# Performance work log

Hardware: AMD Instinct MI355X
Metric: run time of the kernel (lower is better)

Reference implementation:

```python
import jax, jax.numpy as jnp
import numpy as np

HIDDEN = 1024
N_HEADS = 16
HEAD_DIM = 64
BS, QS = 4, 2048
NEG = -60000.0


def setup_inputs() -> dict:
    key = jax.random.key(0)
    k1, k2, k3, k4 = jax.random.split(key, 4)
    x = jax.random.normal(k1, (BS, QS, HIDDEN), dtype=jnp.float32)
    att_mask = jax.random.randint(k2, (BS, QS, QS), 0, 2).astype(bool)
    # nn.Linear(hidden, out, bias=False): store as [in, out] so y = x @ W
    W_qk = jax.random.normal(k3, (HIDDEN, 2 * N_HEADS * HEAD_DIM), dtype=jnp.float32) / np.sqrt(HIDDEN)
    W_v = jax.random.normal(k4, (HIDDEN, N_HEADS), dtype=jnp.float32) / np.sqrt(HIDDEN)
    return {"x": x, "att_mask": att_mask, "W_qk": W_qk, "W_v": W_v}


def reference(x, att_mask, W_qk, W_v):
    # mem is None -> c = x, ks == qs
    bs, qs, _ = x.shape
    n_heads = W_v.shape[1]
    head_dim = W_qk.shape[1] // (2 * n_heads)
    att_scale = 1.0 / head_dim ** 0.5

    qk = x @ W_qk                                   # [b, k, 2*n*d]
    query, key = jnp.split(qk, 2, axis=-1)
    value = x @ W_v                                 # [b, k, n]  (per-head V dim is 1)

    q = query.reshape(bs, qs, n_heads, head_dim)
    k = key.reshape(bs, qs, n_heads, head_dim)

    # att_score: [b, q, k, n]
    scores = jnp.einsum('bqnd,bknd->bqkn', q, k) * att_scale
    scores = jnp.where(att_mask[..., None], NEG, scores)  # True = masked
    prob = jax.nn.softmax(scores, axis=2)           # softmax over k
    # attended bqnd with d=1, then .sum(2) over heads -> [b, q, 1]
    attended = jnp.einsum('bqkn,bkn->bqn', prob, value)
    out = attended.sum(-1, keepdims=True)           # [b, q, 1]

    padded_mask = att_mask[:, -1]                   # [b, k] == [b, q]
    out = jnp.where(padded_mask[..., None], NEG, out)
    out = jax.nn.sigmoid(out)
    # torch version also returns out.nonzero() (data-dependent shape); omitted for jit.
    return out
```

## Files before the change

kernel.cpp:

```cpp
#include <hip/hip_runtime.h>

typedef unsigned short u16;
typedef unsigned int u32;
typedef unsigned long long u64;
typedef __attribute__((ext_vector_type(8))) short bf16x8;
typedef __attribute__((ext_vector_type(4))) float f32x4;

#define BATCH 4
#define SEQ 2048
#define HID 1024
#define NHEAD 16
#define HDIM 64
#define C1 0.18033688011112042f

#if __has_builtin(__builtin_amdgcn_exp2f)
#define EXP2(x) __builtin_amdgcn_exp2f(x)
#else
#define EXP2(x) exp2f(x)
#endif

__device__ __forceinline__ u16 f2bf(float f) {
    u32 u = __builtin_bit_cast(u32, f);
    u += 0x7fffu + ((u >> 16) & 1u);
    return (u16)(u >> 16);
}

__device__ __forceinline__ void gl_lds16(const void* g, void* l) {
    __builtin_amdgcn_global_load_lds((const __attribute__((address_space(1))) u32*)g,
                                     (__attribute__((address_space(3))) u32*)l, 16, 0, 0);
}

__global__ __launch_bounds__(1024) void flagk(const unsigned char* mask, int* flag) {
    __shared__ int any;
    if (threadIdx.x == 0) any = 0;
    __syncthreads();
    const uint4* m4 = (const uint4*)mask;
    u32 acc = 0;
#pragma unroll
    for (int j = 0; j < 4; ++j) {
        uint4 v = m4[threadIdx.x + j * 1024];
        acc |= (v.x | v.y | v.z | v.w) & 0xFFFFFF00u;
    }
    if (acc) atomicOr(&any, 1);
    __syncthreads();
    if (threadIdx.x == 0) *flag = (any == 0) ? 1 : 0;
}

__global__ void convx(const float* __restrict__ x, u16* __restrict__ xb) {
    int i = blockIdx.x * 256 + threadIdx.x;
    float4 v = ((const float4*)x)[i];
    ushort4 o;
    o.x = f2bf(v.x); o.y = f2bf(v.y); o.z = f2bf(v.z); o.w = f2bf(v.w);
    ((ushort4*)xb)[i] = o;
}

__global__ __launch_bounds__(256) void transw(const float* __restrict__ W, u16* __restrict__ wT) {
    __shared__ float t[32][33];
    int nb = blockIdx.x & 63, hb = blockIdx.x >> 6;
    int tx = threadIdx.x & 31, ty = threadIdx.x >> 5;
#pragma unroll
    for (int i = 0; i < 4; ++i)
        t[ty + i * 8][tx] = W[(size_t)(hb * 32 + ty + i * 8) * 2048 + nb * 32 + tx];
    __syncthreads();
#pragma unroll
    for (int i = 0; i < 4; ++i)
        wT[(size_t)(nb * 32 + ty + i * 8) * 1024 + hb * 32 + tx] = f2bf(t[tx][ty + i * 8]);
}

__global__ __launch_bounds__(256) void value_gemm(const float* __restrict__ x,
                                                  const float* __restrict__ Wv,
                                                  float* __restrict__ vT) {
    __shared__ float xs[16 * 1024];
    int s0 = blockIdx.x * 16;
    const float4* xg = (const float4*)(x + (size_t)s0 * HID);
    float4* xd = (float4*)xs;
    for (int i = threadIdx.x; i < 4096; i += 256) xd[i] = xg[i];
    __syncthreads();
    int sl = threadIdx.x >> 4, n = threadIdx.x & 15;
    float acc = 0.f;
    for (int hh = 0; hh < HID; ++hh) acc += xs[sl * HID + hh] * Wv[hh * 16 + n];
    int s = s0 + sl;
    int b = s >> 11, q = s & 2047;
    vT[((size_t)b * 16 + n) * SEQ + q] = acc;
}

__global__ void bitpack(const void* __restrict__ mask, const int* __restrict__ flag,
                        u64* __restrict__ bm) {
    int base = blockIdx.x * 2048 + threadIdx.x;
    int fl = *flag;
#pragma unroll
    for (int k = 0; k < 8; ++k) {
        int i = base + k * 256;
        int v;
        if (fl) v = ((const int*)mask)[i];
        else    v = ((const unsigned char*)mask)[i];
        u64 bits = __ballot(v == 0);
        if ((threadIdx.x & 63) == 0) bm[i >> 6] = bits;
    }
}

__global__ __launch_bounds__(256) void proj_gemm(const u16* __restrict__ xb,
                                                 const u16* __restrict__ wT,
                                                 u16* __restrict__ qkb) {
    __shared__ __align__(16) u16 As[2][128 * 64];
    __shared__ __align__(16) u16 Bs[2][128 * 64];
    int tid = threadIdx.x, w = tid >> 6, lane = tid & 63;
    int g = lane >> 4, l15 = lane & 15;
    int bid = blockIdx.x;
    int swz = (bid & 7) * 128 + (bid >> 3);
    int bm = swz >> 4, bn = swz & 15;
    int m0 = bm * 128, n0 = bn * 128;
    int wm = w >> 1, wn = w & 1;
    const u16* asrc[4];
    const u16* bsrc[4];
#pragma unroll
    for (int j = 0; j < 4; ++j) {
        int ci = (w * 4 + j) * 64 + lane;
        int row = ci >> 3, cl = (ci & 7) ^ (row & 7);
        asrc[j] = xb + (size_t)(m0 + row) * HID + cl * 8;
        bsrc[j] = wT + (size_t)(n0 + row) * HID + cl * 8;
    }
    f32x4 acc[4][4] = {};
#pragma unroll
    for (int j = 0; j < 4; ++j) {
        gl_lds16(asrc[j], &As[0][(w * 4 + j) * 512]);
        gl_lds16(bsrc[j], &Bs[0][(w * 4 + j) * 512]);
        asrc[j] += 64; bsrc[j] += 64;
    }
    for (int kt = 0; kt < 16; ++kt) {
        int cur = kt & 1;
        asm volatile("s_waitcnt vmcnt(0)" ::: "memory");
        __builtin_amdgcn_s_barrier();
        __builtin_amdgcn_sched_barrier(0);
        if (kt < 15) {
#pragma unroll
            for (int j = 0; j < 4; ++j) {
                gl_lds16(asrc[j], &As[cur ^ 1][(w * 4 + j) * 512]);
                gl_lds16(bsrc[j], &Bs[cur ^ 1][(w * 4 + j) * 512]);
                asrc[j] += 64; bsrc[j] += 64;
            }
        }
#pragma unroll
        for (int kk = 0; kk < 2; ++kk) {
            bf16x8 af[4], bf[4];
#pragma unroll
            for (int m = 0; m < 4; ++m) {
                int row = wm * 64 + m * 16 + l15;
                int cp = (kk * 4 + g) ^ (row & 7);
                af[m] = *(const bf16x8*)&As[cur][row * 64 + cp * 8];
            }
#pragma unroll
            for (int n = 0; n < 4; ++n) {
                int row = wn * 64 + n * 16 + l15;
                int cp = (kk * 4 + g) ^ (row & 7);
                bf[n] = *(const bf16x8*)&Bs[cur][row * 64 + cp * 8];
            }
#pragma unroll
            for (int m = 0; m < 4; ++m)
#pragma unroll
                for (int n = 0; n < 4; ++n)
                    acc[m][n] = __builtin_amdgcn_mfma_f32_16x16x32_bf16(af[m], bf[n], acc[m][n], 0, 0, 0);
        }
    }
    float scale = (bn < 8) ? C1 : 1.0f;
#pragma unroll
    for (int m = 0; m < 4; ++m)
#pragma unroll
        for (int n = 0; n < 4; ++n)
#pragma unroll
            for (int r = 0; r < 4; ++r) {
                int row = m0 + wm * 64 + m * 16 + g * 4 + r;
                int col = n0 + wn * 64 + n * 16 + l15;
                qkb[(size_t)row * 2048 + col] = f2bf(acc[m][n][r] * scale);
            }
}

__global__ __launch_bounds__(512, 4) void attn(const u16* __restrict__ qkb,
                                               const float* __restrict__ vT,
                                               const u64* __restrict__ bmk,
                                               float* __restrict__ hatt) {
    __shared__ __align__(16) u16 Ks[3][64 * 64];
    __shared__ __align__(16) float Vh[2048];
    __shared__ __align__(16) float Tb[16][4];
    int tid = threadIdx.x, w = tid >> 6, lane = tid & 63;
    int g = lane >> 4, l15 = lane & 15, g4 = g * 4;
    int bid = blockIdx.x;
    int swzb = (bid & 7) * 64 + (bid >> 3);
    int qt = swzb & 7, h = (swzb >> 3) & 15, b = swzb >> 7;
    int q0 = qt * 256;
    if (tid < 64) Tb[tid >> 2][tid & 3] = (float)(((tid >> 2) >> (tid & 3)) & 1);
    int qA = q0 + w * 32 + l15, qB = qA + 16;
    const u16* qrowA = qkb + (size_t)(b * SEQ + qA) * 2048 + h * 64;
    const u16* qrowB = qkb + (size_t)(b * SEQ + qB) * 2048 + h * 64;
    bf16x8 qfA0 = *(const bf16x8*)(qrowA + g * 8);
    bf16x8 qfA1 = *(const bf16x8*)(qrowA + 32 + g * 8);
    bf16x8 qfB0 = *(const bf16x8*)(qrowB + g * 8);
    bf16x8 qfB1 = *(const bf16x8*)(qrowB + 32 + g * 8);
    gl_lds16(vT + ((size_t)b * 16 + h) * SEQ + tid * 4, &Vh[w * 256]);
    const u64* mrowA = bmk + ((size_t)b * SEQ + qA) * 32;
    const u64* mrowB = bmk + ((size_t)b * SEQ + qB) * 32;
    int srow = tid >> 3, scol = (tid & 7) ^ (srow & 7);
    const u16* ksrc = qkb + (size_t)(b * SEQ + srow) * 2048 + 1024 + h * 64 + scol * 8;
    u64 mA_cur = mrowA[0], mB_cur = mrowB[0];
    gl_lds16(ksrc, &Ks[0][w * 512]); ksrc += 64 * 2048;
    u64 mA_nxt = mrowA[1], mB_nxt = mrowB[1];
    gl_lds16(ksrc, &Ks[1][w * 512]); ksrc += 64 * 2048;
    int e0[4], e1[4];
#pragma unroll
    for (int cb = 0; cb < 4; ++cb) {
        int krow = cb * 16 + l15;
        e0[cb] = krow * 64 + ((g) ^ (krow & 7)) * 8;
        e1[cb] = krow * 64 + ((4 + g) ^ (krow & 7)) * 8;
    }
    float nmA0 = 0.f, nmA1 = 0.f, nmA2 = 0.f, nmA3 = 0.f;
    float dnA0 = 0.f, dnA1 = 0.f, dnA2 = 0.f, dnA3 = 0.f;
    float nmB0 = 0.f, nmB1 = 0.f, nmB2 = 0.f, nmB3 = 0.f;
    float dnB0 = 0.f, dnB1 = 0.f, dnB2 = 0.f, dnB3 = 0.f;
    asm volatile("s_waitcnt lgkmcnt(0)" ::: "memory");

    auto compute = [&](int kt) {
        const u16* kcur = &Ks[kt % 3][0];
        const float* vk = &Vh[kt * 64 + g4];
        u64 shA = mA_cur >> g4, shB = mB_cur >> g4;
        u32 aLo = (u32)shA, aHi = (u32)(shA >> 32);
        u32 bLo = (u32)shB, bHi = (u32)(shB >> 32);
        int idxA[4] = {(int)(aLo & 15), (int)((aLo >> 16) & 15),
                       (int)(aHi & 15), (int)((aHi >> 16) & 15)};
        int idxB[4] = {(int)(bLo & 15), (int)((bLo >> 16) & 15),
                       (int)(bHi & 15), (int)((bHi >> 16) & 15)};
#pragma unroll
        for (int cb = 0; cb < 4; ++cb) {
            bf16x8 kf0 = *(const bf16x8*)&kcur[e0[cb]];
            bf16x8 kf1 = *(const bf16x8*)&kcur[e1[cb]];
            f32x4 aA = {0.f, 0.f, 0.f, 0.f}, aB = {0.f, 0.f, 0.f, 0.f};
            aA = __builtin_amdgcn_mfma_f32_16x16x32_bf16(kf0, qfA0, aA, 0, 0, 0);
            aA = __builtin_amdgcn_mfma_f32_16x16x32_bf16(kf1, qfA1, aA, 0, 0, 0);
            aB = __builtin_amdgcn_mfma_f32_16x16x32_bf16(kf0, qfB0, aB, 0, 0, 0);
            aB = __builtin_amdgcn_mfma_f32_16x16x32_bf16(kf1, qfB1, aB, 0, 0, 0);
            const float4 mA4 = *(const float4*)&Tb[idxA[cb]][0];
            const float4 mB4 = *(const float4*)&Tb[idxB[cb]][0];
            const float4 vv = *(const float4*)&vk[cb * 16];
            float pA0 = EXP2(aA[0]) * mA4.x, pA1 = EXP2(aA[1]) * mA4.y;
            float pA2 = EXP2(aA[2]) * mA4.z, pA3 = EXP2(aA[3]) * mA4.w;
            float pB0 = EXP2(aB[0]) * mB4.x, pB1 = EXP2(aB[1]) * mB4.y;
            float pB2 = EXP2(aB[2]) * mB4.z, pB3 = EXP2(aB[3]) * mB4.w;
            dnA0 += pA0; dnA1 += pA1; dnA2 += pA2; dnA3 += pA3;
            dnB0 += pB0; dnB1 += pB1; dnB2 += pB2; dnB3 += pB3;
            nmA0 = fmaf(pA0, vv.x, nmA0); nmA1 = fmaf(pA1, vv.y, nmA1);
            nmA2 = fmaf(pA2, vv.z, nmA2); nmA3 = fmaf(pA3, vv.w, nmA3);
            nmB0 = fmaf(pB0, vv.x, nmB0); nmB1 = fmaf(pB1, vv.y, nmB1);
            nmB2 = fmaf(pB2, vv.z, nmB2); nmB3 = fmaf(pB3, vv.w, nmB3);
        }
    };

    for (int kt = 0; kt < 31; ++kt) {
        asm volatile("s_waitcnt vmcnt(3)" ::: "memory");
        __builtin_amdgcn_s_barrier();
        __builtin_amdgcn_sched_barrier(0);
        u64 mA_n2, mB_n2;
        if (kt < 30) {
            mA_n2 = mrowA[kt + 2]; mB_n2 = mrowB[kt + 2];
            gl_lds16(ksrc, &Ks[(kt + 2) % 3][w * 512]); ksrc += 64 * 2048;
        } else { mA_n2 = 0; mB_n2 = 0; }
        compute(kt);
        mA_cur = mA_nxt; mB_cur = mB_nxt;
        mA_nxt = mA_n2; mB_nxt = mB_n2;
    }
    asm volatile("s_waitcnt vmcnt(0)" ::: "memory");
    __builtin_amdgcn_s_barrier();
    __builtin_amdgcn_sched_barrier(0);
    compute(31);

    float numA = (nmA0 + nmA1) + (nmA2 + nmA3);
    float denA = (dnA0 + dnA1) + (dnA2 + dnA3);
    float numB = (nmB0 + nmB1) + (nmB2 + nmB3);
    float denB = (dnB0 + dnB1) + (dnB2 + dnB3);
    numA += __shfl_xor(numA, 16); denA += __shfl_xor(denA, 16);
    numA += __shfl_xor(numA, 32); denA += __shfl_xor(denA, 32);
    numB += __shfl_xor(numB, 16); denB += __shfl_xor(denB, 16);
    numB += __shfl_xor(numB, 32); denB += __shfl_xor(denB, 32);
    if (g == 0) {
        hatt[((size_t)b * SEQ + qA) * 16 + h] = numA / denA;
        hatt[((size_t)b * SEQ + qB) * 16 + h] = numB / denB;
    }
}

__global__ void epi(const float* __restrict__ hatt, const void* __restrict__ mask,
                    const int* __restrict__ flag, float* __restrict__ out) {
    int i = blockIdx.x * 256 + threadIdx.x;
    int b = i >> 11, q = i & 2047;
    const float4* hp = (const float4*)(hatt + (size_t)i * 16);
    float t = 0.f;
#pragma unroll
    for (int j = 0; j < 4; ++j) {
        float4 u = hp[j];
        t += u.x + u.y + u.z + u.w;
    }
    size_t mi = ((size_t)b * SEQ + (SEQ - 1)) * SEQ + q;
    int m;
    if (*flag) m = ((const int*)mask)[mi];
    else       m = ((const unsigned char*)mask)[mi];
    out[i] = m ? 0.f : 1.f / (1.f + expf(-t));
}

extern "C" void kernel_launch(void* const* d_in, const int* in_sizes, int n_in,
                              void* d_out, int out_size, void* d_ws, size_t ws_size,
                              hipStream_t stream) {
    const float* x = (const float*)d_in[0];
    const void* mask = d_in[1];
    const float* Wqk = (const float*)d_in[2];
    const float* Wv = (const float*)d_in[3];
    float* out = (float*)d_out;
    char* ws = (char*)d_ws;
    u16* xb = (u16*)(ws + 0);
    u16* wT = (u16*)(ws + 16777216);
    u16* qkb = (u16*)(ws + 20971520);
    float* vT = (float*)(ws + 54525952);
    u64* bm = (u64*)(ws + 55050240);
    float* hatt = (float*)(ws + 0);
    int* flag = (int*)(ws + 57147392);

    flagk<<<1, 1024, 0, stream>>>((const unsigned char*)mask, flag);
    convx<<<8192, 256, 0, stream>>>(x, xb);
    transw<<<2048, 256, 0, stream>>>(Wqk, wT);
    value_gemm<<<512, 256, 0, stream>>>(x, Wv, vT);
    bitpack<<<8192, 256, 0, stream>>>(mask, flag, bm);
    proj_gemm<<<1024, 256, 0, stream>>>(xb, wT, qkb);
    attn<<<512, 512, 0, stream>>>(qkb, vT, bm, hatt);
    epi<<<32, 256, 0, stream>>>(hatt, mask, flag, out);
}
```

Before: 168.3 us.

## Fuse x bf16 conversion with value GEMM and halve attention query tile

After: 170.8 us. No clear change (+1.4%).

```diff
diff --git a/kernel.cpp b/kernel.cpp
--- a/kernel.cpp
+++ b/kernel.cpp
@@ -46,12 +46,36 @@
     if (threadIdx.x == 0) *flag = (any == 0) ? 1 : 0;
 }
 
-__global__ void convx(const float* __restrict__ x, u16* __restrict__ xb) {
-    int i = blockIdx.x * 256 + threadIdx.x;
-    float4 v = ((const float4*)x)[i];
-    ushort4 o;
-    o.x = f2bf(v.x); o.y = f2bf(v.y); o.z = f2bf(v.z); o.w = f2bf(v.w);
-    ((ushort4*)xb)[i] = o;
+__global__ __launch_bounds__(256) void convxv(const float* __restrict__ x,
+                                              const float* __restrict__ Wv,
+                                              u16* __restrict__ xb,
+                                              float* __restrict__ vT) {
+    __shared__ float xs[16 * 1024];
+    int s0 = blockIdx.x * 16;
+    const float4* xg = (const float4*)(x + (size_t)s0 * HID);
+    float4* xd = (float4*)xs;
+    ushort4* xo = (ushort4*)(xb + (size_t)s0 * HID);
+#pragma unroll
+    for (int j = 0; j < 16; ++j) {
+        int i = j * 256 + threadIdx.x;
+        float4 v = xg[i];
+        xd[i] = v;
+        ushort4 o;
+        o.x = f2bf(v.x); o.y = f2bf(v.y); o.z = f2bf(v.z); o.w = f2bf(v.w);
+        xo[i] = o;
+    }
+    __syncthreads();
+    int sl = threadIdx.x >> 4, n = threadIdx.x & 15;
+    const float4* xrow = (const float4*)&xs[sl * HID];
+    float acc = 0.f;
+    for (int h4 = 0; h4 < 256; ++h4) {
+        float4 xv = xrow[h4];
+        acc += xv.x * Wv[(h4 * 4 + 0) * 16 + n] + xv.y * Wv[(h4 * 4 + 1) * 16 + n]
+             + xv.z * Wv[(h4 * 4 + 2) * 16 + n] + xv.w * Wv[(h4 * 4 + 3) * 16 + n];
+    }
+    int s = s0 + sl;
+    int b = s >> 11, q = s & 2047;
+    vT[((size_t)b * 16 + n) * SEQ + q] = acc;
 }
 
 __global__ __launch_bounds__(256) void transw(const float* __restrict__ W, u16* __restrict__ wT) {
@@ -65,23 +89,6 @@
 #pragma unroll
     for (int i = 0; i < 4; ++i)
         wT[(size_t)(nb * 32 + ty + i * 8) * 1024 + hb * 32 + tx] = f2bf(t[tx][ty + i * 8]);
-}
-
-__global__ __launch_bounds__(256) void value_gemm(const float* __restrict__ x,
-                                                  const float* __restrict__ Wv,
-                                                  float* __restrict__ vT) {
-    __shared__ float xs[16 * 1024];
-    int s0 = blockIdx.x * 16;
-    const float4* xg = (const float4*)(x + (size_t)s0 * HID);
-    float4* xd = (float4*)xs;
-    for (int i = threadIdx.x; i < 4096; i += 256) xd[i] = xg[i];
-    __syncthreads();
-    int sl = threadIdx.x >> 4, n = threadIdx.x & 15;
-    float acc = 0.f;
-    for (int hh = 0; hh < HID; ++hh) acc += xs[sl * HID + hh] * Wv[hh * 16 + n];
-    int s = s0 + sl;
-    int b = s >> 11, q = s & 2047;
-    vT[((size_t)b * 16 + n) * SEQ + q] = acc;
 }
 
 __global__ void bitpack(const void* __restrict__ mask, const int* __restrict__ flag,
@@ -185,25 +192,21 @@
     int tid = threadIdx.x, w = tid >> 6, lane = tid & 63;
     int g = lane >> 4, l15 = lane & 15, g4 = g * 4;
     int bid = blockIdx.x;
-    int swzb = (bid & 7) * 64 + (bid >> 3);
-    int qt = swzb & 7, h = (swzb >> 3) & 15, b = swzb >> 7;
-    int q0 = qt * 256;
+    int bh = bid & 63, qt = bid >> 6;
+    int h = bh & 15, b = bh >> 4;
+    int q0 = qt * 128;
     if (tid < 64) Tb[tid >> 2][tid & 3] = (float)(((tid >> 2) >> (tid & 3)) & 1);
-    int qA = q0 + w * 32 + l15, qB = qA + 16;
-    const u16* qrowA = qkb + (size_t)(b * SEQ + qA) * 2048 + h * 64;
-    const u16* qrowB = qkb + (size_t)(b * SEQ + qB) * 2048 + h * 64;
-    bf16x8 qfA0 = *(const bf16x8*)(qrowA + g * 8);
-    bf16x8 qfA1 = *(const bf16x8*)(qrowA + 32 + g * 8);
-    bf16x8 qfB0 = *(const bf16x8*)(qrowB + g * 8);
-    bf16x8 qfB1 = *(const bf16x8*)(qrowB + 32 + g * 8);
+    int q = q0 + w * 16 + l15;
+    const u16* qrow = qkb + (size_t)(b * SEQ + q) * 2048 + h * 64;
+    bf16x8 qf0 = *(const bf16x8*)(qrow + g * 8);
+    bf16x8 qf1 = *(const bf16x8*)(qrow + 32 + g * 8);
     gl_lds16(vT + ((size_t)b * 16 + h) * SEQ + tid * 4, &Vh[w * 256]);
-    const u64* mrowA = bmk + ((size_t)b * SEQ + qA) * 32;
-    const u64* mrowB = bmk + ((size_t)b * SEQ + qB) * 32;
+    const u64* mrow = bmk + ((size_t)b * SEQ + q) * 32;
     int srow = tid >> 3, scol = (tid & 7) ^ (srow & 7);
     const u16* ksrc = qkb + (size_t)(b * SEQ + srow) * 2048 + 1024 + h * 64 + scol * 8;
-    u64 mA_cur = mrowA[0], mB_cur = mrowB[0];
+    u64 m_cur = mrow[0];
     gl_lds16(ksrc, &Ks[0][w * 512]); ksrc += 64 * 2048;
-    u64 mA_nxt = mrowA[1], mB_nxt = mrowB[1];
+    u64 m_nxt = mrow[1];
     gl_lds16(ksrc, &Ks[1][w * 512]); ksrc += 64 * 2048;
     int e0[4], e1[4];
 #pragma unroll
@@ -212,77 +215,61 @@
         e0[cb] = krow * 64 + ((g) ^ (krow & 7)) * 8;
         e1[cb] = krow * 64 + ((4 + g) ^ (krow & 7)) * 8;
     }
-    float nmA0 = 0.f, nmA1 = 0.f, nmA2 = 0.f, nmA3 = 0.f;
-    float dnA0 = 0.f, dnA1 = 0.f, dnA2 = 0.f, dnA3 = 0.f;
-    float nmB0 = 0.f, nmB1 = 0.f, nmB2 = 0.f, nmB3 = 0.f;
-    float dnB0 = 0.f, dnB1 = 0.f, dnB2 = 0.f, dnB3 = 0.f;
-    asm volatile("s_waitcnt lgkmcnt(0)" ::: "memory");
+    float nm0 = 0.f, nm1 = 0.f, nm2 = 0.f, nm3 = 0.f;
+    float dn0 = 0.f, dn1 = 0.f, dn2 = 0.f, dn3 = 0.f;
+    asm volatile("s_waitcnt vmcnt(0) lgkmcnt(0)" ::: "memory");
+    __builtin_amdgcn_s_barrier();
 
     auto compute = [&](int kt) {
         const u16* kcur = &Ks[kt % 3][0];
         const float* vk = &Vh[kt * 64 + g4];
-        u64 shA = mA_cur >> g4, shB = mB_cur >> g4;
-        u32 aLo = (u32)shA, aHi = (u32)(shA >> 32);
-        u32 bLo = (u32)shB, bHi = (u32)(shB >> 32);
-        int idxA[4] = {(int)(aLo & 15), (int)((aLo >> 16) & 15),
-                       (int)(aHi & 15), (int)((aHi >> 16) & 15)};
-        int idxB[4] = {(int)(bLo & 15), (int)((bLo >> 16) & 15),
-                       (int)(bHi & 15), (int)((bHi >> 16) & 15)};
+        u64 sh = m_cur >> g4;
+        u32 mlo = (u32)sh, mhi = (u32)(sh >> 32);
+        int idx[4] = {(int)(mlo & 15), (int)((mlo >> 16) & 15),
+                      (int)(mhi & 15), (int)((mhi >> 16) & 15)};
 #pragma unroll
         for (int cb = 0; cb < 4; ++cb) {
             bf16x8 kf0 = *(const bf16x8*)&kcur[e0[cb]];
             bf16x8 kf1 = *(const bf16x8*)&kcur[e1[cb]];
-            f32x4 aA = {0.f, 0.f, 0.f, 0.f}, aB = {0.f, 0.f, 0.f, 0.f};
-            aA = __builtin_amdgcn_mfma_f32_16x16x32_bf16(kf0, qfA0, aA, 0, 0, 0);
-            aA = __builtin_amdgcn_mfma_f32_16x16x32_bf16(kf1, qfA1, aA, 0, 0, 0);
-            aB = __builtin_amdgcn_mfma_f32_16x16x32_bf16(kf0, qfB0, aB, 0, 0, 0);
-            aB = __builtin_amdgcn_mfma_f32_16x16x32_bf16(kf1, qfB1, aB, 0, 0, 0);
-            const float4 mA4 = *(const float4*)&Tb[idxA[cb]][0];
-            const float4 mB4 = *(const float4*)&Tb[idxB[cb]][0];
+            f32x4 a = {0.f, 0.f, 0.f, 0.f};
+            a = __builtin_amdgcn_mfma_f32_16x16x32_bf16(kf0, qf0, a, 0, 0, 0);
+            a = __builtin_amdgcn_mfma_f32_16x16x32_bf16(kf1, qf1, a, 0, 0, 0);
+            const float4 m4 = *(const float4*)&Tb[idx[cb]][0];
             const float4 vv = *(const float4*)&vk[cb * 16];
-            float pA0 = EXP2(aA[0]) * mA4.x, pA1 = EXP2(aA[1]) * mA4.y;
-            float pA2 = EXP2(aA[2]) * mA4.z, pA3 = EXP2(aA[3]) * mA4.w;
-            float pB0 = EXP2(aB[0]) * mB4.x, pB1 = EXP2(aB[1]) * mB4.y;
-            float pB2 = EXP2(aB[2]) * mB4.z, pB3 = EXP2(aB[3]) * mB4.w;
-            dnA0 += pA0; dnA1 += pA1; dnA2 += pA2; dnA3 += pA3;
-            dnB0 += pB0; dnB1 += pB1; dnB2 += pB2; dnB3 += pB3;
-            nmA0 = fmaf(pA0, vv.x, nmA0); nmA1 = fmaf(pA1, vv.y, nmA1);
-            nmA2 = fmaf(pA2, vv.z, nmA2); nmA3 = fmaf(pA3, vv.w, nmA3);
-            nmB0 = fmaf(pB0, vv.x, nmB0); nmB1 = fmaf(pB1, vv.y, nmB1);
-            nmB2 = fmaf(pB2, vv.z, nmB2); nmB3 = fmaf(pB3, vv.w, nmB3);
+            float p0 = EXP2(a[0]) * m4.x;
+            float p1 = EXP2(a[1]) * m4.y;
+            float p2 = EXP2(a[2]) * m4.z;
+            float p3 = EXP2(a[3]) * m4.w;
+            dn0 += p0; dn1 += p1; dn2 += p2; dn3 += p3;
+            nm0 = fmaf(p0, vv.x, nm0);
+            nm1 = fmaf(p1, vv.y, nm1);
+            nm2 = fmaf(p2, vv.z, nm2);
+            nm3 = fmaf(p3, vv.w, nm3);
         }
     };
 
     for (int kt = 0; kt < 31; ++kt) {
-        asm volatile("s_waitcnt vmcnt(3)" ::: "memory");
+        asm volatile("s_waitcnt vmcnt(2)" ::: "memory");
         __builtin_amdgcn_s_barrier();
         __builtin_amdgcn_sched_barrier(0);
-        u64 mA_n2, mB_n2;
+        u64 m_n2 = 0;
         if (kt < 30) {
-            mA_n2 = mrowA[kt + 2]; mB_n2 = mrowB[kt + 2];
+            m_n2 = mrow[kt + 2];
             gl_lds16(ksrc, &Ks[(kt + 2) % 3][w * 512]); ksrc += 64 * 2048;
-        } else { mA_n2 = 0; mB_n2 = 0; }
+        }
         compute(kt);
-        mA_cur = mA_nxt; mB_cur = mB_nxt;
-        mA_nxt = mA_n2; mB_nxt = mB_n2;
+        m_cur = m_nxt; m_nxt = m_n2;
     }
     asm volatile("s_waitcnt vmcnt(0)" ::: "memory");
     __builtin_amdgcn_s_barrier();
     __builtin_amdgcn_sched_barrier(0);
     compute(31);
 
-    float numA = (nmA0 + nmA1) + (nmA2 + nmA3);
-    float denA = (dnA0 + dnA1) + (dnA2 + dnA3);
-    float numB = (nmB0 + nmB1) + (nmB2 + nmB3);
-    float denB = (dnB0 + dnB1) + (dnB2 + dnB3);
-    numA += __shfl_xor(numA, 16); denA += __shfl_xor(denA, 16);
-    numA += __shfl_xor(numA, 32); denA += __shfl_xor(denA, 32);
-    numB += __shfl_xor(numB, 16); denB += __shfl_xor(denB, 16);
-    numB += __shfl_xor(numB, 32); denB += __shfl_xor(denB, 32);
-    if (g == 0) {
-        hatt[((size_t)b * SEQ + qA) * 16 + h] = numA / denA;
-        hatt[((size_t)b * SEQ + qB) * 16 + h] = numB / denB;
-    }
+    float num = (nm0 + nm1) + (nm2 + nm3);
+    float den = (dn0 + dn1) + (dn2 + dn3);
+    num += __shfl_xor(num, 16); den += __shfl_xor(den, 16);
+    num += __shfl_xor(num, 32); den += __shfl_xor(den, 32);
+    if (g == 0) hatt[((size_t)b * SEQ + q) * 16 + h] = num / den;
 }
 
 __global__ void epi(const float* __restrict__ hatt, const void* __restrict__ mask,
@@ -321,11 +308,10 @@
     int* flag = (int*)(ws + 57147392);
 
     flagk<<<1, 1024, 0, stream>>>((const unsigned char*)mask, flag);
-    convx<<<8192, 256, 0, stream>>>(x, xb);
+    convxv<<<512, 256, 0, stream>>>(x, Wv, xb, vT);
     transw<<<2048, 256, 0, stream>>>(Wqk, wT);
-    value_gemm<<<512, 256, 0, stream>>>(x, Wv, vT);
     bitpack<<<8192, 256, 0, stream>>>(mask, flag, bm);
     proj_gemm<<<1024, 256, 0, stream>>>(xb, wT, qkb);
-    attn<<<512, 512, 0, stream>>>(qkb, vT, bm, hatt);
+    attn<<<1024, 512, 0, stream>>>(qkb, vT, bm, hatt);
     epi<<<32, 256, 0, stream>>>(hatt, mask, flag, out);
 }
```

## Fuse bf16 conversion with value GEMM; load K directly to registers in attention

Applied to the files above, without the earlier changes.

New measurement: 379.7 us. 126% more time.

```diff
diff --git a/kernel.cpp b/kernel.cpp
--- a/kernel.cpp
+++ b/kernel.cpp
@@ -46,12 +46,36 @@
     if (threadIdx.x == 0) *flag = (any == 0) ? 1 : 0;
 }
 
-__global__ void convx(const float* __restrict__ x, u16* __restrict__ xb) {
-    int i = blockIdx.x * 256 + threadIdx.x;
-    float4 v = ((const float4*)x)[i];
-    ushort4 o;
-    o.x = f2bf(v.x); o.y = f2bf(v.y); o.z = f2bf(v.z); o.w = f2bf(v.w);
-    ((ushort4*)xb)[i] = o;
+__global__ __launch_bounds__(256) void convxv(const float* __restrict__ x,
+                                              const float* __restrict__ Wv,
+                                              u16* __restrict__ xb,
+                                              float* __restrict__ vT) {
+    __shared__ float xs[16 * 1024];
+    int s0 = blockIdx.x * 16;
+    const float4* xg = (const float4*)(x + (size_t)s0 * HID);
+    float4* xd = (float4*)xs;
+    ushort4* xo = (ushort4*)(xb + (size_t)s0 * HID);
+#pragma unroll
+    for (int j = 0; j < 16; ++j) {
+        int i = j * 256 + threadIdx.x;
+        float4 v = xg[i];
+        xd[i] = v;
+        ushort4 o;
+        o.x = f2bf(v.x); o.y = f2bf(v.y); o.z = f2bf(v.z); o.w = f2bf(v.w);
+        xo[i] = o;
+    }
+    __syncthreads();
+    int sl = threadIdx.x >> 4, n = threadIdx.x & 15;
+    const float4* xrow = (const float4*)&xs[sl * HID];
+    float acc = 0.f;
+    for (int h4 = 0; h4 < 256; ++h4) {
+        float4 xv = xrow[h4];
+        acc += xv.x * Wv[(h4 * 4 + 0) * 16 + n] + xv.y * Wv[(h4 * 4 + 1) * 16 + n]
+             + xv.z * Wv[(h4 * 4 + 2) * 16 + n] + xv.w * Wv[(h4 * 4 + 3) * 16 + n];
+    }
+    int s = s0 + sl;
+    int b = s >> 11, q = s & 2047;
+    vT[((size_t)b * 16 + n) * SEQ + q] = acc;
 }
 
 __global__ __launch_bounds__(256) void transw(const float* __restrict__ W, u16* __restrict__ wT) {
@@ -65,23 +89,6 @@
 #pragma unroll
     for (int i = 0; i < 4; ++i)
         wT[(size_t)(nb * 32 + ty + i * 8) * 1024 + hb * 32 + tx] = f2bf(t[tx][ty + i * 8]);
-}
-
-__global__ __launch_bounds__(256) void value_gemm(const float* __restrict__ x,
-                                                  const float* __restrict__ Wv,
-                                                  float* __restrict__ vT) {
-    __shared__ float xs[16 * 1024];
-    int s0 = blockIdx.x * 16;
-    const float4* xg = (const float4*)(x + (size_t)s0 * HID);
-    float4* xd = (float4*)xs;
-    for (int i = threadIdx.x; i < 4096; i += 256) xd[i] = xg[i];
-    __syncthreads();
-    int sl = threadIdx.x >> 4, n = threadIdx.x & 15;
-    float acc = 0.f;
-    for (int hh = 0; hh < HID; ++hh) acc += xs[sl * HID + hh] * Wv[hh * 16 + n];
-    int s = s0 + sl;
-    int b = s >> 11, q = s & 2047;
-    vT[((size_t)b * 16 + n) * SEQ + q] = acc;
 }
 
 __global__ void bitpack(const void* __restrict__ mask, const int* __restrict__ flag,
@@ -175,20 +182,23 @@
             }
 }
 
-__global__ __launch_bounds__(512, 4) void attn(const u16* __restrict__ qkb,
+__global__ __launch_bounds__(256, 3) void attn(const u16* __restrict__ qkb,
                                                const float* __restrict__ vT,
                                                const u64* __restrict__ bmk,
                                                float* __restrict__ hatt) {
-    __shared__ __align__(16) u16 Ks[3][64 * 64];
     __shared__ __align__(16) float Vh[2048];
     __shared__ __align__(16) float Tb[16][4];
     int tid = threadIdx.x, w = tid >> 6, lane = tid & 63;
     int g = lane >> 4, l15 = lane & 15, g4 = g * 4;
     int bid = blockIdx.x;
-    int swzb = (bid & 7) * 64 + (bid >> 3);
-    int qt = swzb & 7, h = (swzb >> 3) & 15, b = swzb >> 7;
-    int q0 = qt * 256;
+    int c = bid & 7, r = bid >> 3;
+    int bh = c * 8 + (r & 7), qt = r >> 3;
+    int h = bh & 15, b = bh >> 4;
+    int q0 = qt * 128;
     if (tid < 64) Tb[tid >> 2][tid & 3] = (float)(((tid >> 2) >> (tid & 3)) & 1);
+    const float* vsrc = vT + ((size_t)b * 16 + h) * SEQ;
+    gl_lds16(vsrc + (size_t)tid * 4, &Vh[w * 256]);
+    gl_lds16(vsrc + 1024 + (size_t)tid * 4, &Vh[1024 + w * 256]);
     int qA = q0 + w * 32 + l15, qB = qA + 16;
     const u16* qrowA = qkb + (size_t)(b * SEQ + qA) * 2048 + h * 64;
     const u16* qrowB = qkb + (size_t)(b * SEQ + qB) * 2048 + h * 64;
@@ -196,32 +206,29 @@
     bf16x8 qfA1 = *(const bf16x8*)(qrowA + 32 + g * 8);
     bf16x8 qfB0 = *(const bf16x8*)(qrowB + g * 8);
     bf16x8 qfB1 = *(const bf16x8*)(qrowB + 32 + g * 8);
-    gl_lds16(vT + ((size_t)b * 16 + h) * SEQ + tid * 4, &Vh[w * 256]);
     const u64* mrowA = bmk + ((size_t)b * SEQ + qA) * 32;
     const u64* mrowB = bmk + ((size_t)b * SEQ + qB) * 32;
-    int srow = tid >> 3, scol = (tid & 7) ^ (srow & 7);
-    const u16* ksrc = qkb + (size_t)(b * SEQ + srow) * 2048 + 1024 + h * 64 + scol * 8;
-    u64 mA_cur = mrowA[0], mB_cur = mrowB[0];
-    gl_lds16(ksrc, &Ks[0][w * 512]); ksrc += 64 * 2048;
-    u64 mA_nxt = mrowA[1], mB_nxt = mrowB[1];
-    gl_lds16(ksrc, &Ks[1][w * 512]); ksrc += 64 * 2048;
-    int e0[4], e1[4];
-#pragma unroll
-    for (int cb = 0; cb < 4; ++cb) {
-        int krow = cb * 16 + l15;
-        e0[cb] = krow * 64 + ((g) ^ (krow & 7)) * 8;
-        e1[cb] = krow * 64 + ((4 + g) ^ (krow & 7)) * 8;
-    }
+    const u16* kbase = qkb + (size_t)(b * SEQ) * 2048 + 1024 + h * 64;
+
+    auto loadK = [&](bf16x8* kf, int kt) {
+        const u16* kb = kbase + (size_t)kt * 64 * 2048;
+#pragma unroll
+        for (int cb = 0; cb < 4; ++cb) {
+            const u16* kr = kb + (size_t)(cb * 16 + l15) * 2048 + g * 8;
+            kf[cb * 2]     = *(const bf16x8*)kr;
+            kf[cb * 2 + 1] = *(const bf16x8*)(kr + 32);
+        }
+    };
+
     float nmA0 = 0.f, nmA1 = 0.f, nmA2 = 0.f, nmA3 = 0.f;
     float dnA0 = 0.f, dnA1 = 0.f, dnA2 = 0.f, dnA3 = 0.f;
     float nmB0 = 0.f, nmB1 = 0.f, nmB2 = 0.f, nmB3 = 0.f;
     float dnB0 = 0.f, dnB1 = 0.f, dnB2 = 0.f, dnB3 = 0.f;
-    asm volatile("s_waitcnt lgkmcnt(0)" ::: "memory");
-
-    auto compute = [&](int kt) {
-        const u16* kcur = &Ks[kt % 3][0];
+
+    auto compute = [&](const bf16x8* kf, int kt) {
+        u64 mwA = mrowA[kt], mwB = mrowB[kt];
         const float* vk = &Vh[kt * 64 + g4];
-        u64 shA = mA_cur >> g4, shB = mB_cur >> g4;
+        u64 shA = mwA >> g4, shB = mwB >> g4;
         u32 aLo = (u32)shA, aHi = (u32)(shA >> 32);
         u32 bLo = (u32)shB, bHi = (u32)(shB >> 32);
         int idxA[4] = {(int)(aLo & 15), (int)((aLo >> 16) & 15),
@@ -230,13 +237,11 @@
                        (int)(bHi & 15), (int)((bHi >> 16) & 15)};
 #pragma unroll
         for (int cb = 0; cb < 4; ++cb) {
-            bf16x8 kf0 = *(const bf16x8*)&kcur[e0[cb]];
-            bf16x8 kf1 = *(const bf16x8*)&kcur[e1[cb]];
             f32x4 aA = {0.f, 0.f, 0.f, 0.f}, aB = {0.f, 0.f, 0.f, 0.f};
-            aA = __builtin_amdgcn_mfma_f32_16x16x32_bf16(kf0, qfA0, aA, 0, 0, 0);
-            aA = __builtin_amdgcn_mfma_f32_16x16x32_bf16(kf1, qfA1, aA, 0, 0, 0);
-            aB = __builtin_amdgcn_mfma_f32_16x16x32_bf16(kf0, qfB0, aB, 0, 0, 0);
-            aB = __builtin_amdgcn_mfma_f32_16x16x32_bf16(kf1, qfB1, aB, 0, 0, 0);
+            aA = __builtin_amdgcn_mfma_f32_16x16x32_bf16(kf[cb * 2], qfA0, aA, 0, 0, 0);
+            aA = __builtin_amdgcn_mfma_f32_16x16x32_bf16(kf[cb * 2 + 1], qfA1, aA, 0, 0, 0);
+            aB = __builtin_amdgcn_mfma_f32_16x16x32_bf16(kf[cb * 2], qfB0, aB, 0, 0, 0);
+            aB = __builtin_amdgcn_mfma_f32_16x16x32_bf16(kf[cb * 2 + 1], qfB1, aB, 0, 0, 0);
             const float4 mA4 = *(const float4*)&Tb[idxA[cb]][0];
             const float4 mB4 = *(const float4*)&Tb[idxB[cb]][0];
             const float4 vv = *(const float4*)&vk[cb * 16];
@@ -253,23 +258,15 @@
         }
     };
 
-    for (int kt = 0; kt < 31; ++kt) {
-        asm volatile("s_waitcnt vmcnt(3)" ::: "memory");
-        __builtin_amdgcn_s_barrier();
-        __builtin_amdgcn_sched_barrier(0);
-        u64 mA_n2, mB_n2;
-        if (kt < 30) {
-            mA_n2 = mrowA[kt + 2]; mB_n2 = mrowB[kt + 2];
-            gl_lds16(ksrc, &Ks[(kt + 2) % 3][w * 512]); ksrc += 64 * 2048;
-        } else { mA_n2 = 0; mB_n2 = 0; }
-        compute(kt);
-        mA_cur = mA_nxt; mB_cur = mB_nxt;
-        mA_nxt = mA_n2; mB_nxt = mB_n2;
-    }
-    asm volatile("s_waitcnt vmcnt(0)" ::: "memory");
-    __builtin_amdgcn_s_barrier();
-    __builtin_amdgcn_sched_barrier(0);
-    compute(31);
+    bf16x8 kfA[8], kfB[8];
+    loadK(kfA, 0);
+    __syncthreads();
+    for (int kt = 0; kt < 32; kt += 2) {
+        loadK(kfB, kt + 1);
+        compute(kfA, kt);
+        if (kt + 2 < 32) loadK(kfA, kt + 2);
+        compute(kfB, kt + 1);
+    }
 
     float numA = (nmA0 + nmA1) + (nmA2 + nmA3);
     float denA = (dnA0 + dnA1) + (dnA2 + dnA3);
@@ -321,11 +318,10 @@
     int* flag = (int*)(ws + 57147392);
 
     flagk<<<1, 1024, 0, stream>>>((const unsigned char*)mask, flag);
-    convx<<<8192, 256, 0, stream>>>(x, xb);
+    convxv<<<512, 256, 0, stream>>>(x, Wv, xb, vT);
     transw<<<2048, 256, 0, stream>>>(Wqk, wT);
-    value_gemm<<<512, 256, 0, stream>>>(x, Wv, vT);
     bitpack<<<8192, 256, 0, stream>>>(mask, flag, bm);
     proj_gemm<<<1024, 256, 0, stream>>>(xb, wT, qkb);
-    attn<<<512, 512, 0, stream>>>(qkb, vT, bm, hatt);
+    attn<<<1024, 256, 0, stream>>>(qkb, vT, bm, hatt);
     epi<<<32, 256, 0, stream>>>(hatt, mask, flag, out);
 }
```
